# Optimization experiments

Hardware: AMD Instinct MI355X
Metric: run time of the kernel (lower is better)

Reference implementation:

```python
import jax, jax.numpy as jnp
import numpy as np
from functools import partial

NEG_INF = -1e30

def _alive_mask(x, umbral=0.1):
    # 3x3 max-pool (stride 1, SAME) over channel 0, compare to threshold
    m = x[..., :1]
    pooled = jax.lax.reduce_window(m, NEG_INF, jax.lax.max,
                                   (1, 3, 3, 1), (1, 1, 1, 1), 'SAME')
    return pooled > umbral

def _perception_kernel(canales):
    # identity + sobel-x + sobel-y, fixed (non-learned) depthwise filters
    identidad = np.outer(np.float32([0, 1, 0]), np.float32([0, 1, 0]))
    dx = np.float32(np.outer([1, 2, 1], [-1, 0, 1]) / 8.0)
    dy = dx.T
    k = np.stack([identidad, dx, dy], -1)            # [3,3,3]
    k = np.repeat(k[:, :, None, :], canales + 3, 2)   # [3,3,C+3,3]
    C = canales + 3
    # TF depthwise output channel order: chan*3 + multiplier -> flatten last two dims
    return jnp.asarray(k.reshape(3, 3, 1, C * 3))

def setup_inputs() -> dict:
    key = jax.random.key(0)
    ks = jax.random.split(key, 6)
    B, H, C, HID = 16, 256, 14, 256
    PERC = (C + 3) * 3  # 51
    x = jax.random.uniform(ks[0], (B, H, H, C), dtype=jnp.float32)
    imagen = jax.random.uniform(ks[1], (H, H, 3), dtype=jnp.float32)
    W1 = jax.random.normal(ks[2], (PERC, HID), dtype=jnp.float32) * 0.05
    b1 = jnp.zeros((HID,), dtype=jnp.float32)
    W2 = jax.random.normal(ks[3], (HID, C), dtype=jnp.float32) * 0.05
    b2 = jnp.zeros((C,), dtype=jnp.float32)
    return {"x": x, "imagen": imagen, "W1": W1, "b1": b1, "W2": W2, "b2": b2}

def reference(x, imagen, W1, b1, W2, b2):
    paso = 0.1
    umbral_actualizacion = 0.5
    B = x.shape[0]
    C = x.shape[-1]

    vivos_antes = _alive_mask(x)

    # percibir: concat image, fixed depthwise conv (identity/sobel)
    img_b = jnp.broadcast_to(imagen[None], (B,) + imagen.shape)
    xc = jnp.concatenate([x, img_b], axis=3)                 # [B,H,W,C+3]
    kernel = _perception_kernel(C)                            # [3,3,1,(C+3)*3]
    perc = jax.lax.conv_general_dilated(
        xc, kernel, window_strides=(1, 1), padding='SAME',
        dimension_numbers=('NHWC', 'HWIO', 'NHWC'),
        feature_group_count=C + 3)                            # [B,H,W,51]

    # pointwise MLP (1x1 convs)
    h = jax.nn.relu(jnp.einsum('bhwc,cd->bhwd', perc, W1) + b1)
    dx = (jnp.einsum('bhwd,dc->bhwc', h, W2) + b2) * paso

    # stochastic update mask
    mk = jax.random.fold_in(jax.random.key(0), 1234)
    upd = jax.random.uniform(mk, x[..., :1].shape) <= umbral_actualizacion
    x = x + dx * upd.astype(jnp.float32)

    vivos = jnp.logical_and(vivos_antes, _alive_mask(x))
    return x * vivos.astype(jnp.float32)
```

## Files before the change

kernel.cpp:

```cpp
#include <hip/hip_runtime.h>
#include <stdint.h>

#define C    14
#define CX   17
#define PERC 51
#define HID  256

typedef __attribute__((ext_vector_type(4))) short  bf16x4;
typedef __attribute__((ext_vector_type(8))) short  bf16x8;
typedef __attribute__((ext_vector_type(4))) float  f32x4;
typedef __attribute__((ext_vector_type(8))) unsigned short u16x8;
typedef __attribute__((ext_vector_type(2))) uint32_t u32x2;

__device__ __forceinline__ float bfu(unsigned short u) {
  return __uint_as_float(((uint32_t)u) << 16);
}
__device__ __forceinline__ unsigned short bf16r(float f) {
  uint32_t u = __float_as_uint(f);
  return (unsigned short)((u + 0x7fffu + ((u >> 16) & 1u)) >> 16);
}
__device__ __forceinline__ uint32_t pack2_bf16(float lo, float hi) {
  const uint32_t ul = __float_as_uint(lo) + 0x8000u;
  const uint32_t uh = __float_as_uint(hi) + 0x8000u;
#if __has_builtin(__builtin_amdgcn_perm)
  return __builtin_amdgcn_perm(uh, ul, 0x07060302u);
#else
  return (uh & 0xffff0000u) | (ul >> 16);
#endif
}
__device__ __forceinline__ unsigned short pack1_bf16(float f) {
  return (unsigned short)((__float_as_uint(f) + 0x8000u) >> 16);
}

__device__ __forceinline__ f32x4 mfma32(bf16x8 a, bf16x8 b, f32x4 c) {
  return __builtin_amdgcn_mfma_f32_16x16x32_bf16(a, b, c, 0, 0, 0);
}
#if __has_builtin(__builtin_amdgcn_mfma_f32_16x16x16bf16_1k)
#define HAVE_MFMA16_BUILTIN 1
#endif
__device__ __forceinline__ f32x4 mfma16(bf16x4 a, bf16x4 b, f32x4 c) {
#ifdef HAVE_MFMA16_BUILTIN
  return __builtin_amdgcn_mfma_f32_16x16x16bf16_1k(a, b, c, 0, 0, 0);
#else
  asm volatile("v_mfma_f32_16x16x16_bf16 %0, %1, %2, %0" : "+v"(c) : "v"(a), "v"(b));
  return c;
#endif
}

__device__ __forceinline__ void tf_round(uint32_t& x0, uint32_t& x1, int r) {
  x0 += x1; x1 = (x1 << r) | (x1 >> (32 - r)); x1 ^= x0;
}
__device__ __forceinline__ void threefry2x32(uint32_t k0, uint32_t k1,
                                             uint32_t& x0, uint32_t& x1) {
  const uint32_t ks2 = k0 ^ k1 ^ 0x1BD11BDAu;
  x0 += k0; x1 += k1;
  tf_round(x0,x1,13); tf_round(x0,x1,15); tf_round(x0,x1,26); tf_round(x0,x1,6);
  x0 += k1; x1 += ks2 + 1u;
  tf_round(x0,x1,17); tf_round(x0,x1,29); tf_round(x0,x1,16); tf_round(x0,x1,24);
  x0 += ks2; x1 += k0 + 2u;
  tf_round(x0,x1,13); tf_round(x0,x1,15); tf_round(x0,x1,26); tf_round(x0,x1,6);
  x0 += k0; x1 += k1 + 3u;
  tf_round(x0,x1,17); tf_round(x0,x1,29); tf_round(x0,x1,16); tf_round(x0,x1,24);
  x0 += k1; x1 += ks2 + 4u;
  tf_round(x0,x1,13); tf_round(x0,x1,15); tf_round(x0,x1,26); tf_round(x0,x1,6);
  x0 += ks2; x1 += k0 + 5u;
}
__device__ __forceinline__ float upd_val(uint32_t gpix) {
  uint32_t fk0 = 0u, fk1 = 1234u;
  threefry2x32(0u, 0u, fk0, fk1);
  uint32_t a = 0u, b = gpix;
  threefry2x32(fk0, fk1, a, b);
  const uint32_t bits = a ^ b;
  const float u = __uint_as_float((bits >> 9) | 0x3f800000u) - 1.0f;
  return (u <= 0.5f) ? 1.0f : 0.0f;
}

__global__ void nca_prep(const float* __restrict__ W1, const float* __restrict__ b1,
                         const float* __restrict__ W2, const float* __restrict__ b2,
                         unsigned short* __restrict__ w1fu,
                         unsigned short* __restrict__ w2fu,
                         float* __restrict__ b2p) {
  const int bid = blockIdx.x, t = threadIdx.x;
  if (bid < 64) {
    const int f = bid * 256 + t;
    const int j = f & 7, l = (f >> 3) & 63, k2 = (f >> 9) & 1, mt = f >> 10;
    const int n = mt * 16 + (l & 15);
    const int k = k2 * 32 + ((l >> 4) & 3) * 8 + j;
    float v = 0.0f;
    if (k < PERC)       v = W1[k * HID + n];
    else if (k == PERC) v = b1[n];
    w1fu[f] = bf16r(v);
  } else if (bid < 80) {
    const int f = (bid - 64) * 256 + t;
    const int j = f & 3, l = (f >> 2) & 63, ks = f >> 8;
    const int co = l & 15;
    const int k = ks * 16 + ((l >> 4) & 3) * 4 + j;
    const float v = (co < C) ? W2[k * C + co] : 0.0f;
    w2fu[f] = bf16r(v);
  } else if (t < 16) {
    b2p[t] = (t < C) ? b2[t] : 0.0f;
  }
}

__global__ __launch_bounds__(256, 4)
void nca_main(const float* __restrict__ x, const float* __restrict__ img,
              const unsigned short* __restrict__ w1fu,
              const unsigned short* __restrict__ w2fu,
              const float* __restrict__ b2p,
              float* __restrict__ out, float* __restrict__ plane) {
  __shared__ union {
    unsigned short xcs[18 * 18 * 24];
    unsigned short Ps[256 * 64];
  } sh;
  __shared__ float updf[256];

  const int t    = threadIdx.x;
  const int bid  = blockIdx.x;
  const int bb   = bid >> 8;
  const int tile = bid & 255;
  const int row0 = (tile >> 4) << 4, col0 = (tile & 15) << 4;

  for (int e = t; e < 324; e += 256) {
    const int r = e / 18, c = e - r * 18;
    const int gr = row0 + r - 1, gc = col0 + c - 1;
    uint32_t w[8]; unsigned short w16;
    if ((unsigned)gr < 256u && (unsigned)gc < 256u) {
      const size_t gp = (size_t)bb * 65536 + (size_t)gr * 256 + gc;
      const float* xp = x + gp * C;
      float v[17];
      #pragma unroll
      for (int k = 0; k < 7; ++k) {
        const float2 f2 = *(const float2*)(xp + 2 * k);
        v[2 * k] = f2.x; v[2 * k + 1] = f2.y;
      }
      const float* ip = img + ((size_t)gr * 256 + gc) * 3;
      v[14] = ip[0]; v[15] = ip[1]; v[16] = ip[2];
      #pragma unroll
      for (int k = 0; k < 8; ++k)
        w[k] = pack2_bf16(v[2 * k], v[2 * k + 1]);
      w16 = pack1_bf16(v[16]);
    } else {
      #pragma unroll
      for (int k = 0; k < 8; ++k) w[k] = 0u;
      w16 = 0;
    }
    uint32_t* d = (uint32_t*)&sh.xcs[e * 24];
    #pragma unroll
    for (int k = 0; k < 8; ++k) d[k] = w[k];
    sh.xcs[e * 24 + 16] = w16;
  }

  {
    const uint32_t g = ((uint32_t)bb * 256u + (uint32_t)(row0 + (t >> 4))) * 256u
                       + (uint32_t)(col0 + (t & 15));
    updf[t] = upd_val(g);
  }
  __syncthreads();

  const int pr = t >> 4, pc = t & 15;
  float pe[64];
  #pragma unroll
  for (int h = 0; h < 2; ++h) {
    u16x8 nb[9];
    #pragma unroll
    for (int i = 0; i < 3; ++i)
      #pragma unroll
      for (int j = 0; j < 3; ++j)
        nb[i * 3 + j] = *(const u16x8*)&sh.xcs[((pr + i) * 18 + (pc + j)) * 24 + h * 8];
    #pragma unroll
    for (int cc = 0; cc < 8; ++cc) {
      const int ch = h * 8 + cc;
      const float a00 = bfu(nb[0][cc]), a01 = bfu(nb[1][cc]), a02 = bfu(nb[2][cc]);
      const float a10 = bfu(nb[3][cc]), a11 = bfu(nb[4][cc]), a12 = bfu(nb[5][cc]);
      const float a20 = bfu(nb[6][cc]), a21 = bfu(nb[7][cc]), a22 = bfu(nb[8][cc]);
      pe[3 * ch + 0] = a11;
      pe[3 * ch + 1] = ((a02 - a00) + 2.0f * (a12 - a10) + (a22 - a20)) * 0.125f;
      pe[3 * ch + 2] = ((a20 - a00) + 2.0f * (a21 - a01) + (a22 - a02)) * 0.125f;
    }
  }
  {
    float a[9];
    #pragma unroll
    for (int i = 0; i < 3; ++i)
      #pragma unroll
      for (int j = 0; j < 3; ++j)
        a[i * 3 + j] = bfu(sh.xcs[((pr + i) * 18 + (pc + j)) * 24 + 16]);
    pe[48] = a[4];
    pe[49] = ((a[2] - a[0]) + 2.0f * (a[5] - a[3]) + (a[8] - a[6])) * 0.125f;
    pe[50] = ((a[6] - a[0]) + 2.0f * (a[7] - a[1]) + (a[8] - a[2])) * 0.125f;
  }
  pe[51] = 1.0f;
  #pragma unroll
  for (int k = 52; k < 64; ++k) pe[k] = 0.0f;

  __syncthreads();

  #pragma unroll
  for (int g = 0; g < 8; ++g) {
    uint4 v;
    v.x = pack2_bf16(pe[g * 8 + 0], pe[g * 8 + 1]);
    v.y = pack2_bf16(pe[g * 8 + 2], pe[g * 8 + 3]);
    v.z = pack2_bf16(pe[g * 8 + 4], pe[g * 8 + 5]);
    v.w = pack2_bf16(pe[g * 8 + 6], pe[g * 8 + 7]);
    *(uint4*)&sh.Ps[(t << 6) + ((g ^ (t & 7)) << 3)] = v;
  }
  __syncthreads();

  const int lane = t & 63;
  const int wv   = t >> 6;
  const int wbase = wv << 6;
  const int lg = lane >> 4;
  const int lc = lane & 15;

  bf16x8 bF0[4], bF1[4];
  #pragma unroll
  for (int nt = 0; nt < 4; ++nt) {
    const int pix = wbase + nt * 16 + lc;
    bF0[nt] = *(const bf16x8*)&sh.Ps[(pix << 6) + ((lg ^ (pix & 7)) << 3)];
    bF1[nt] = *(const bf16x8*)&sh.Ps[(pix << 6) + (((4 + lg) ^ (pix & 7)) << 3)];
  }

  f32x4 dxacc[4];
  {
    const float4 b2v = *(const float4*)(b2p + lg * 4);
    #pragma unroll
    for (int nt = 0; nt < 4; ++nt)
      dxacc[nt] = (f32x4){b2v.x, b2v.y, b2v.z, b2v.w};
  }

  #pragma unroll
  for (int nc = 0; nc < 4; ++nc) {
    bf16x8 aF[4][2];
    #pragma unroll
    for (int m4 = 0; m4 < 4; ++m4)
      #pragma unroll
      for (int k2 = 0; k2 < 2; ++k2)
        aF[m4][k2] = *(const bf16x8*)(w1fu + (((((nc * 4 + m4) * 2 + k2) * 64) + lane) << 3));

    f32x4 acc[4][4];
    #pragma unroll
    for (int m4 = 0; m4 < 4; ++m4)
      #pragma unroll
      for (int nt = 0; nt < 4; ++nt)
        acc[m4][nt] = (f32x4){0.0f, 0.0f, 0.0f, 0.0f};

    #pragma unroll
    for (int nt = 0; nt < 4; ++nt) {
      #pragma unroll
      for (int m4 = 0; m4 < 4; ++m4) acc[m4][nt] = mfma32(aF[m4][0], bF0[nt], acc[m4][nt]);
      #pragma unroll
      for (int m4 = 0; m4 < 4; ++m4) acc[m4][nt] = mfma32(aF[m4][1], bF1[nt], acc[m4][nt]);
    }

    #pragma unroll
    for (int m4 = 0; m4 < 4; ++m4) {
      const bf16x4 wf = *(const bf16x4*)(w2fu + ((((nc * 4 + m4) * 64) + lane) << 2));
      #pragma unroll
      for (int nt = 0; nt < 4; ++nt) {
        u32x2 pw;
        pw.x = pack2_bf16(fmaxf(acc[m4][nt][0], 0.0f), fmaxf(acc[m4][nt][1], 0.0f));
        pw.y = pack2_bf16(fmaxf(acc[m4][nt][2], 0.0f), fmaxf(acc[m4][nt][3], 0.0f));
        dxacc[nt] = mfma16(wf, __builtin_bit_cast(bf16x4, pw), dxacc[nt]);
      }
    }
  }
#ifndef HAVE_MFMA16_BUILTIN
  asm volatile("s_nop 7\n\ts_nop 7" :::);
#endif

  #pragma unroll
  for (int nt = 0; nt < 4; ++nt) {
    const int pix = wbase + nt * 16 + lc;
    const float sc = 0.1f * updf[pix];
    const int gr = row0 + (pix >> 4), gc = col0 + (pix & 15);
    const size_t gp = (size_t)bb * 65536 + (size_t)gr * 256 + gc;
    const float* xp = x + gp * C + lg * 4;
    float* op = out + gp * C + lg * 4;
    const f32x4 d = dxacc[nt];
    if (lg < 3) {
      const float2 u0 = *(const float2*)xp;
      const float2 u1 = *(const float2*)(xp + 2);
      const float r0 = u0.x + d[0] * sc, r1 = u0.y + d[1] * sc;
      const float r2 = u1.x + d[2] * sc, r3 = u1.y + d[3] * sc;
      *(float2*)op = make_float2(r0, r1);
      *(float2*)(op + 2) = make_float2(r2, r3);
      if (lg == 0) plane[gp] = r0;
    } else {
      const float2 u0 = *(const float2*)xp;
      *(float2*)op = make_float2(u0.x + d[0] * sc, u0.y + d[1] * sc);
    }
  }
}

__global__ __launch_bounds__(256)
void nca_mask(const float* __restrict__ x, const float* __restrict__ plane,
              float* __restrict__ out) {
  __shared__ float sN[18 * 18];
  __shared__ float sO[18 * 18];
  const int t    = threadIdx.x;
  const int bid  = blockIdx.x;
  const int bb   = bid >> 8;
  const int tile = bid & 255;
  const int row0 = (tile >> 4) << 4, col0 = (tile & 15) << 4;

  for (int e = t; e < 18 * 18; e += 256) {
    const int r = e / 18, c = e - r * 18;
    const int gr = row0 + r - 1, gc = col0 + c - 1;
    float vn = 0.0f, vo = 0.0f;
    if ((unsigned)gr < 256u && (unsigned)gc < 256u) {
      const size_t gp = ((size_t)bb * 256 + gr) * 256 + gc;
      vn = plane[gp];
      vo = x[gp * C];
    }
    sN[e] = vn; sO[e] = vo;
  }
  __syncthreads();

  const int pr = t >> 4, pc = t & 15;
  float mn = -1e30f, mo = -1e30f;
  #pragma unroll
  for (int i = 0; i < 3; ++i)
    #pragma unroll
    for (int j = 0; j < 3; ++j) {
      mn = fmaxf(mn, sN[(pr + i) * 18 + pc + j]);
      mo = fmaxf(mo, sO[(pr + i) * 18 + pc + j]);
    }
  const bool alive = (mo > 0.1f) && (mn > 0.1f);
  if (!alive) {
    const size_t gp = ((size_t)bb * 256 + row0 + pr) * 256 + col0 + pc;
    float* __restrict__ o = out + gp * C;
    const float2 z = make_float2(0.0f, 0.0f);
    #pragma unroll
    for (int k = 0; k < 7; ++k) ((float2*)o)[k] = z;
  }
}

extern "C" void kernel_launch(void* const* d_in, const int* in_sizes, int n_in,
                              void* d_out, int out_size, void* d_ws, size_t ws_size,
                              hipStream_t stream) {
  const float* x  = (const float*)d_in[0];
  const float* im = (const float*)d_in[1];
  const float* W1 = (const float*)d_in[2];
  const float* b1 = (const float*)d_in[3];
  const float* W2 = (const float*)d_in[4];
  const float* b2 = (const float*)d_in[5];
  float* out   = (float*)d_out;
  float* plane = (float*)d_ws;
  unsigned short* w1fu = (unsigned short*)((char*)d_ws + 4194304);
  unsigned short* w2fu = (unsigned short*)((char*)d_ws + 4194304 + 32768);
  float* b2p = (float*)((char*)d_ws + 4194304 + 32768 + 8192);

  nca_prep<<<81,   256, 0, stream>>>(W1, b1, W2, b2, w1fu, w2fu, b2p);
  nca_main<<<4096, 256, 0, stream>>>(x, im, w1fu, w2fu, b2p, out, plane);
  nca_mask<<<4096, 256, 0, stream>>>(x, plane, out);
}
```

Before: 93.89 us.

## Pack alive thresholds into byte plane and prefetch W1 fragments across chunks

```diff
diff --git a/kernel.cpp b/kernel.cpp
--- a/kernel.cpp
+++ b/kernel.cpp
@@ -107,7 +107,7 @@
               const unsigned short* __restrict__ w1fu,
               const unsigned short* __restrict__ w2fu,
               const float* __restrict__ b2p,
-              float* __restrict__ out, float* __restrict__ plane) {
+              float* __restrict__ out, uint8_t* __restrict__ bplane) {
   __shared__ union {
     unsigned short xcs[18 * 18 * 24];
     unsigned short Ps[256 * 64];
@@ -204,7 +204,6 @@
     v.w = pack2_bf16(pe[g * 8 + 6], pe[g * 8 + 7]);
     *(uint4*)&sh.Ps[(t << 6) + ((g ^ (t & 7)) << 3)] = v;
   }
-  __syncthreads();
 
   const int lane = t & 63;
   const int wv   = t >> 6;
@@ -212,6 +211,15 @@
   const int lg = lane >> 4;
   const int lc = lane & 15;
 
+  bf16x8 aFc[4][2];
+  #pragma unroll
+  for (int m4 = 0; m4 < 4; ++m4)
+    #pragma unroll
+    for (int k2 = 0; k2 < 2; ++k2)
+      aFc[m4][k2] = *(const bf16x8*)(w1fu + ((((m4 * 2 + k2) * 64) + lane) << 3));
+
+  __syncthreads();
+
   bf16x8 bF0[4], bF1[4];
   #pragma unroll
   for (int nt = 0; nt < 4; ++nt) {
@@ -230,12 +238,14 @@
 
   #pragma unroll
   for (int nc = 0; nc < 4; ++nc) {
-    bf16x8 aF[4][2];
-    #pragma unroll
-    for (int m4 = 0; m4 < 4; ++m4)
-      #pragma unroll
-      for (int k2 = 0; k2 < 2; ++k2)
-        aF[m4][k2] = *(const bf16x8*)(w1fu + (((((nc * 4 + m4) * 2 + k2) * 64) + lane) << 3));
+    bf16x8 aFn[4][2];
+    if (nc < 3) {
+      #pragma unroll
+      for (int m4 = 0; m4 < 4; ++m4)
+        #pragma unroll
+        for (int k2 = 0; k2 < 2; ++k2)
+          aFn[m4][k2] = *(const bf16x8*)(w1fu + ((((((nc + 1) * 4 + m4) * 2 + k2) * 64) + lane) << 3));
+    }
 
     f32x4 acc[4][4];
     #pragma unroll
@@ -247,9 +257,9 @@
     #pragma unroll
     for (int nt = 0; nt < 4; ++nt) {
       #pragma unroll
-      for (int m4 = 0; m4 < 4; ++m4) acc[m4][nt] = mfma32(aF[m4][0], bF0[nt], acc[m4][nt]);
-      #pragma unroll
-      for (int m4 = 0; m4 < 4; ++m4) acc[m4][nt] = mfma32(aF[m4][1], bF1[nt], acc[m4][nt]);
+      for (int m4 = 0; m4 < 4; ++m4) acc[m4][nt] = mfma32(aFc[m4][0], bF0[nt], acc[m4][nt]);
+      #pragma unroll
+      for (int m4 = 0; m4 < 4; ++m4) acc[m4][nt] = mfma32(aFc[m4][1], bF1[nt], acc[m4][nt]);
     }
 
     #pragma unroll
@@ -262,6 +272,14 @@
         pw.y = pack2_bf16(fmaxf(acc[m4][nt][2], 0.0f), fmaxf(acc[m4][nt][3], 0.0f));
         dxacc[nt] = mfma16(wf, __builtin_bit_cast(bf16x4, pw), dxacc[nt]);
       }
+    }
+
+    if (nc < 3) {
+      #pragma unroll
+      for (int m4 = 0; m4 < 4; ++m4)
+        #pragma unroll
+        for (int k2 = 0; k2 < 2; ++k2)
+          aFc[m4][k2] = aFn[m4][k2];
     }
   }
 #ifndef HAVE_MFMA16_BUILTIN
@@ -284,7 +302,9 @@
       const float r2 = u1.x + d[2] * sc, r3 = u1.y + d[3] * sc;
       *(float2*)op = make_float2(r0, r1);
       *(float2*)(op + 2) = make_float2(r2, r3);
-      if (lg == 0) plane[gp] = r0;
+      if (lg == 0) {
+        bplane[gp] = (uint8_t)((u0.x > 0.1f ? 1 : 0) | (r0 > 0.1f ? 2 : 0));
+      }
     } else {
       const float2 u0 = *(const float2*)xp;
       *(float2*)op = make_float2(u0.x + d[0] * sc, u0.y + d[1] * sc);
@@ -293,40 +313,32 @@
 }
 
 __global__ __launch_bounds__(256)
-void nca_mask(const float* __restrict__ x, const float* __restrict__ plane,
-              float* __restrict__ out) {
-  __shared__ float sN[18 * 18];
-  __shared__ float sO[18 * 18];
+void nca_mask(const uint8_t* __restrict__ bp, float* __restrict__ out) {
+  __shared__ uint8_t sb[18 * 18];
   const int t    = threadIdx.x;
   const int bid  = blockIdx.x;
   const int bb   = bid >> 8;
   const int tile = bid & 255;
   const int row0 = (tile >> 4) << 4, col0 = (tile & 15) << 4;
 
-  for (int e = t; e < 18 * 18; e += 256) {
+  for (int e = t; e < 324; e += 256) {
     const int r = e / 18, c = e - r * 18;
     const int gr = row0 + r - 1, gc = col0 + c - 1;
-    float vn = 0.0f, vo = 0.0f;
-    if ((unsigned)gr < 256u && (unsigned)gc < 256u) {
-      const size_t gp = ((size_t)bb * 256 + gr) * 256 + gc;
-      vn = plane[gp];
-      vo = x[gp * C];
-    }
-    sN[e] = vn; sO[e] = vo;
+    uint8_t v = 0;
+    if ((unsigned)gr < 256u && (unsigned)gc < 256u)
+      v = bp[(size_t)bb * 65536 + (size_t)gr * 256 + gc];
+    sb[e] = v;
   }
   __syncthreads();
 
   const int pr = t >> 4, pc = t & 15;
-  float mn = -1e30f, mo = -1e30f;
+  int m = 0;
   #pragma unroll
   for (int i = 0; i < 3; ++i)
     #pragma unroll
-    for (int j = 0; j < 3; ++j) {
-      mn = fmaxf(mn, sN[(pr + i) * 18 + pc + j]);
-      mo = fmaxf(mo, sO[(pr + i) * 18 + pc + j]);
-    }
-  const bool alive = (mo > 0.1f) && (mn > 0.1f);
-  if (!alive) {
+    for (int j = 0; j < 3; ++j)
+      m |= sb[(pr + i) * 18 + pc + j];
+  if ((m & 3) != 3) {
     const size_t gp = ((size_t)bb * 256 + row0 + pr) * 256 + col0 + pc;
     float* __restrict__ o = out + gp * C;
     const float2 z = make_float2(0.0f, 0.0f);
@@ -345,12 +357,12 @@
   const float* W2 = (const float*)d_in[4];
   const float* b2 = (const float*)d_in[5];
   float* out   = (float*)d_out;
-  float* plane = (float*)d_ws;
-  unsigned short* w1fu = (unsigned short*)((char*)d_ws + 4194304);
-  unsigned short* w2fu = (unsigned short*)((char*)d_ws + 4194304 + 32768);
-  float* b2p = (float*)((char*)d_ws + 4194304 + 32768 + 8192);
+  uint8_t* bplane = (uint8_t*)d_ws;
+  unsigned short* w1fu = (unsigned short*)((char*)d_ws + 1048576);
+  unsigned short* w2fu = (unsigned short*)((char*)d_ws + 1048576 + 32768);
+  float* b2p = (float*)((char*)d_ws + 1048576 + 32768 + 8192);
 
   nca_prep<<<81,   256, 0, stream>>>(W1, b1, W2, b2, w1fu, w2fu, b2p);
-  nca_main<<<4096, 256, 0, stream>>>(x, im, w1fu, w2fu, b2p, out, plane);
-  nca_mask<<<4096, 256, 0, stream>>>(x, plane, out);
-}
+  nca_main<<<4096, 256, 0, stream>>>(x, im, w1fu, w2fu, b2p, out, bplane);
+  nca_mask<<<4096, 256, 0, stream>>>(bplane, out);
+}
```

Result: faster. 90.97 us (-3.1%).
